# Kernel optimization log

Measured on AMD Instinct MI355X. Metric: run time of the kernel, lower is better.

Reference implementation:

```python
import jax, jax.numpy as jnp
import numpy as np

B, T = 8, 32
DSENS, DA = 512, 32
DS = DE = DIM = 128  # dim_structure = dim_encoded_sensory = memory dim


def l2norm(x, eps=1e-12):
    return x / jnp.maximum(jnp.linalg.norm(x, axis=-1, keepdims=True), eps)


def mlp3(x, W1, b1, W2, b2, W3, b3):
    h = jax.nn.relu(x @ W1 + b1)
    h = jax.nn.relu(h @ W2 + b2)
    return h @ W3 + b3


def mse(a, b):
    return jnp.mean((a - b) ** 2)


def assoc_scan(x, gate, prev):
    # h_t = gate_t * h_{t-1} + x_t with h_0 = prev.  x:[b,t,w], gate:[b,t,1], prev:[b,w]
    x = x.at[:, 0].add(gate[:, 0] * prev)
    def combine(ca, cb):
        ga, xa = ca
        gb, xb = cb
        return ga * gb, xb + gb * xa
    _, h = jax.lax.associative_scan(combine, (gate, x), axis=1)
    return h


def _forward(sensory, actions, enc_w, dec_w, pi_w1, pi_b1, pi_w2, pi_b2, pi_w3, pi_b3,
             rnn_init_hidden, wq, wk, wv, w_hp, m_w1, m_b1, m_w2, m_b2, m_w3, m_b3,
             o_w1, o_b1, o_w2, o_b2, o_w3, o_b3, v_w1, v_b1, v_w2, v_b2, v_w3, v_b3,
             integration_ratio):
    b, t = actions.shape[:2]
    # --- path integration: action MLP -> per-step transition matrices -> sequential RNN scan ---
    trans = mlp3(actions, pi_w1, pi_b1, pi_w2, pi_b2, pi_w3, pi_b3).reshape(b, t, DS, DS)
    h0 = jnp.broadcast_to(l2norm(rnn_init_hidden)[0], (b, DS))
    def step(h, Tm):
        h = l2norm(jax.nn.relu(jnp.einsum('bi,bij->bj', h, Tm)))
        return h, h
    _, hs = jax.lax.scan(step, h0, jnp.moveaxis(trans, 1, 0))
    structural = jnp.moveaxis(hs, 0, 1)                      # [b,t,DS]

    enc = sensory @ enc_w                                    # [b,t,DE]
    meta_p = (m_w1, m_b1, m_w2, m_b2, m_w3, m_b3)

    def retrieve(s, e):
        q = jnp.concatenate([s, e], axis=-1) @ wq            # to_queries
        r = mlp3(q, *meta_p)                                 # meta_memory_mlp (slow copy)
        d = mlp3(r, o_w1, o_b1, o_w2, o_b2, o_w3, o_b3)      # memory_output_decoder
        return d[..., :DS], d[..., DS:]

    dec_gen_s, dec_enc = retrieve(structural, jnp.zeros_like(enc))
    gen_loss = mse(sensory, dec_enc @ dec_w)
    dec_s2, _ = retrieve(jnp.zeros_like(structural), enc)
    relational_loss = 2.0 * mse(dec_s2, structural)          # source computes the identical loss twice
    corr_s, corr_e = retrieve(dec_gen_s, enc)
    sse = jnp.sum((corr_e - enc) ** 2, axis=-1, keepdims=True)
    pred_var = mlp3(jnp.concatenate([corr_s, dec_gen_s, sse], axis=-1),
                    v_w1, v_b1, v_w2, v_b2, v_w3, v_b3)
    inf_s = dec_gen_s + (corr_s - dec_gen_s) * jax.nn.sigmoid(integration_ratio) * pred_var
    consistency_loss = mse(dec_gen_s, inf_s)
    final_s, inf_e = retrieve(inf_s, jnp.zeros_like(enc))
    inf_loss = mse(sensory, inf_e @ dec_w)

    # --- test-time-training memory write: per-sample meta-grads + two assoc scans ---
    joint = jnp.concatenate([final_s, enc], axis=-1)         # [b,t,2*DS]
    keys, values = joint @ wk, joint @ wv                    # [b,t,DIM]
    hp = joint @ w_hp                                        # [b,t,3]
    lr, forget, beta = hp[..., 0], hp[..., 1], hp[..., 2]

    def meta_loss(p, k, v):
        return jnp.mean((mlp3(k, *p) - v) ** 2)
    pb = tuple(jnp.broadcast_to(p, (b,) + p.shape) for p in meta_p)
    grads = jax.vmap(jax.vmap(jax.grad(meta_loss), in_axes=(None, 0, 0)))(pb, keys, values)
    G = jnp.concatenate([g.reshape(b, t, -1) for g in grads], axis=-1)  # [b,t,Wtot]
    W = G.shape[-1]
    p_flat = jnp.broadcast_to(jnp.concatenate([p.ravel() for p in meta_p])[None], (b, W))
    update = assoc_scan(G * lr[..., None], jax.nn.sigmoid(beta)[..., None],
                        jnp.zeros((b, W), G.dtype))          # momentum scan
    acc = assoc_scan(-update, jax.nn.sigmoid(forget)[..., None], p_flat)  # weight-decay scan
    next_state = jnp.concatenate([acc[:, -1], update[:, -1]], axis=-1)    # [b,2W]

    total = gen_loss + relational_loss + consistency_loss + inf_loss
    return jnp.concatenate([jnp.reshape(total, (1,)), next_state.ravel()])


def setup_inputs() -> dict:
    key = jax.random.key(0)
    ks = iter(jax.random.split(key, 48))
    def rn(shape, s=1.0):
        return jax.random.normal(next(ks), shape, dtype=jnp.float32) * s
    def lin(fi, fo):
        return rn((fi, fo), 1.0 / np.sqrt(fi))
    z = lambda n: jnp.zeros((n,), jnp.float32)
    return {
        "sensory": rn((B, T, DSENS)),
        "actions": rn((B, T, DA)),
        "enc_w": lin(DSENS, DE), "dec_w": lin(DE, DSENS),
        "pi_w1": lin(DA, 4 * DA), "pi_b1": z(4 * DA),
        "pi_w2": lin(4 * DA, 4 * DA), "pi_b2": z(4 * DA),
        "pi_w3": lin(4 * DA, DS * DS), "pi_b3": z(DS * DS),
        "rnn_init_hidden": rn((1, DS), 0.01),
        "wq": lin(DS + DE, DIM), "wk": lin(DS + DE, DIM), "wv": lin(DS + DE, DIM),
        "w_hp": lin(DS + DE, 3),
        "m_w1": lin(DIM, 2 * DIM), "m_b1": z(2 * DIM),
        "m_w2": lin(2 * DIM, 2 * DIM), "m_b2": z(2 * DIM),
        "m_w3": lin(2 * DIM, DIM), "m_b3": z(DIM),
        "o_w1": lin(DIM, 2 * DIM), "o_b1": z(2 * DIM),
        "o_w2": lin(2 * DIM, 2 * DIM), "o_b2": z(2 * DIM),
        "o_w3": lin(2 * DIM, DS + DE), "o_b3": z(DS + DE),
        "v_w1": lin(2 * DS + 1, 2 * DS), "v_b1": z(2 * DS),
        "v_w2": lin(2 * DS, 2 * DS), "v_b2": z(2 * DS),
        "v_w3": lin(2 * DS, DS), "v_b3": z(DS),
        "integration_ratio": jnp.zeros((), jnp.float32),
    }


def reference(sensory, actions, enc_w, dec_w, pi_w1, pi_b1, pi_w2, pi_b2, pi_w3, pi_b3,
              rnn_init_hidden, wq, wk, wv, w_hp, m_w1, m_b1, m_w2, m_b2, m_w3, m_b3,
              o_w1, o_b1, o_w2, o_b2, o_w3, o_b3, v_w1, v_b1, v_w2, v_b2, v_w3, v_b3,
              integration_ratio):
    return _forward(sensory, actions, enc_w, dec_w, pi_w1, pi_b1, pi_w2, pi_b2, pi_w3, pi_b3,
                    rnn_init_hidden, wq, wk, wv, w_hp, m_w1, m_b1, m_w2, m_b2, m_w3, m_b3,
                    o_w1, o_b1, o_w2, o_b2, o_w3, o_b3, v_w1, v_b1, v_w2, v_b2, v_w3, v_b3,
                    integration_ratio)
```

## Files before the change

kernel.cpp:

```cpp
#include <hip/hip_runtime.h>
#include <cstdint>
#include <cstddef>

#define DEV __device__ __forceinline__

constexpr size_t W_TOT = 131712;
constexpr size_t OFF_W1 = 0;
constexpr size_t OFF_B1 = 32768;
constexpr size_t OFF_W2 = 33024;
constexpr size_t OFF_B2 = 98560;
constexpr size_t OFF_W3 = 98816;
constexpr size_t OFF_B3 = 131584;

constexpr int OPS = 272;

constexpr size_t P_LOSS = 0;
constexpr size_t P_WA   = 1024;
constexpr size_t P_WU   = 1280;
constexpr size_t P_FT   = 1536;
constexpr size_t P_HP   = 2048;
constexpr size_t P_H2PI = 4096;
constexpr size_t P_ENC  = P_H2PI + 32768;
constexpr size_t P_DGS  = P_ENC + 32768;
constexpr size_t P_INF  = P_DGS + 32768;
constexpr size_t P_KEYS = P_INF + 32768;
constexpr size_t P_VALS = P_KEYS + 32768;
constexpr size_t P_D3   = P_VALS + 32768;
constexpr size_t P_H1   = P_D3 + 32768;
constexpr size_t P_H2   = P_H1 + 65536;
constexpr size_t P_D1   = P_H2 + 65536;
constexpr size_t P_D2   = P_D1 + 65536;
constexpr size_t P_STRUCT = P_D2 + 65536;
constexpr size_t P_TRANS  = P_STRUCT + 32768;

DEV float sigm(float x) { return 1.f / (1.f + expf(-x)); }

DEV float wgsum256(float v, float* red) {
#pragma unroll
  for (int s = 32; s > 0; s >>= 1) v += __shfl_xor(v, s);
  if ((threadIdx.x & 63) == 0) red[threadIdx.x >> 6] = v;
  __syncthreads();
  const float t = red[0] + red[1] + red[2] + red[3];
  __syncthreads();
  return t;
}

template<int K, int OUT, int ROWS>
DEV void denseV4(const float* __restrict__ W, const float* __restrict__ bias,
                 const float* in, int ips, float* out, int ops, int relu,
                 float* scr)
{
  constexpr int OUTG = OUT / 4;
  constexpr int NSEG = 256 / OUTG;
  constexpr int KS = K / NSEG;
  constexpr int NG = KS / 8;
  static_assert(KS % 8 == 0 && NG >= 2, "bad shape");
  const int tid = (int)threadIdx.x;
  const int c = tid & (OUTG - 1);
  const int seg = tid / OUTG;
  const int k0 = seg * KS;
  const float4* W4 = reinterpret_cast<const float4*>(W);
  float4 w0[8], w1[8];
  float acc[ROWS][4];
#pragma unroll
  for (int r = 0; r < ROWS; ++r)
#pragma unroll
    for (int x = 0; x < 4; ++x) acc[r][x] = 0.f;
#pragma unroll
  for (int u = 0; u < 8; ++u) w0[u] = W4[(size_t)(k0 + u) * OUTG + c];
#pragma unroll
  for (int t = 1; t <= NG; ++t) {
    if (t < NG) {
#pragma unroll
      for (int u = 0; u < 8; ++u) w1[u] = W4[(size_t)(k0 + t * 8 + u) * OUTG + c];
    }
#pragma unroll
    for (int u = 0; u < 8; ++u) {
      const int kk = k0 + (t - 1) * 8 + u;
#pragma unroll
      for (int r = 0; r < ROWS; ++r) {
        const float x = in[r * ips + kk];
        acc[r][0] = fmaf(x, w0[u].x, acc[r][0]);
        acc[r][1] = fmaf(x, w0[u].y, acc[r][1]);
        acc[r][2] = fmaf(x, w0[u].z, acc[r][2]);
        acc[r][3] = fmaf(x, w0[u].w, acc[r][3]);
      }
    }
    if (t < NG) {
#pragma unroll
      for (int u = 0; u < 8; ++u) w0[u] = w1[u];
    }
  }
  float4* scr4 = reinterpret_cast<float4*>(scr);
#pragma unroll
  for (int r = 0; r < ROWS; ++r)
    scr4[(seg * ROWS + r) * OUTG + c] =
        make_float4(acc[r][0], acc[r][1], acc[r][2], acc[r][3]);
  __syncthreads();
  for (int idx = tid; idx < OUT * ROWS; idx += 256) {
    const int r = idx / OUT, j = idx % OUT;
    float v = (bias ? bias[j] : 0.f);
#pragma unroll
    for (int s = 0; s < NSEG; ++s) v += scr[(s * ROWS + r) * OUT + j];
    if (relu) v = fmaxf(v, 0.f);
    out[r * ops + j] = v;
  }
  __syncthreads();
}

DEV float declossV4(const float* de, const float* __restrict__ dec_w,
                    const float* sens, float* scr)
{
  const int tid = (int)threadIdx.x;
  const int c = tid & 127;
  const int seg = tid >> 7;
  const int k0 = seg * 64;
  const float4* W4 = reinterpret_cast<const float4*>(dec_w);
  float4 w0[8], w1[8];
  float a[4] = { 0.f, 0.f, 0.f, 0.f };
#pragma unroll
  for (int u = 0; u < 8; ++u) w0[u] = W4[(size_t)(k0 + u) * 128 + c];
#pragma unroll
  for (int t = 1; t <= 8; ++t) {
    if (t < 8) {
#pragma unroll
      for (int u = 0; u < 8; ++u) w1[u] = W4[(size_t)(k0 + t * 8 + u) * 128 + c];
    }
#pragma unroll
    for (int u = 0; u < 8; ++u) {
      const float x = de[k0 + (t - 1) * 8 + u];
      a[0] = fmaf(x, w0[u].x, a[0]);
      a[1] = fmaf(x, w0[u].y, a[1]);
      a[2] = fmaf(x, w0[u].z, a[2]);
      a[3] = fmaf(x, w0[u].w, a[3]);
    }
    if (t < 8) {
#pragma unroll
      for (int u = 0; u < 8; ++u) w0[u] = w1[u];
    }
  }
  float4* scr4 = reinterpret_cast<float4*>(scr);
  scr4[seg * 128 + c] = make_float4(a[0], a[1], a[2], a[3]);
  __syncthreads();
  float lsum = 0.f;
  for (int j = tid; j < 512; j += 256) {
    const float v = scr[j] + scr[512 + j];
    const float d = v - sens[j];
    lsum = fmaf(d, d, lsum);
  }
  __syncthreads();
  return lsum;
}

__global__ __launch_bounds__(128) void k_pi_h2(
    const float* __restrict__ actions,
    const float* __restrict__ w1, const float* __restrict__ b1,
    const float* __restrict__ w2, const float* __restrict__ b2,
    float* __restrict__ h2out)
{
  const int row = blockIdx.x;
  const int j = threadIdx.x;
  __shared__ float a[32];
  __shared__ float h1[128];
  if (j < 32) a[j] = actions[row * 32 + j];
  __syncthreads();
  float acc = b1[j];
#pragma unroll
  for (int i = 0; i < 32; ++i) acc = fmaf(a[i], w1[i * 128 + j], acc);
  h1[j] = fmaxf(acc, 0.f);
  __syncthreads();
  float acc2 = b2[j];
#pragma unroll 8
  for (int i = 0; i < 128; ++i) acc2 = fmaf(h1[i], w2[i * 128 + j], acc2);
  h2out[row * 128 + j] = fmaxf(acc2, 0.f);
}

__global__ __launch_bounds__(256) void k_pi_trans(
    const float* __restrict__ h2,
    const float* __restrict__ w3, const float* __restrict__ b3,
    float* __restrict__ trans)
{
  const int col = blockIdx.x * 256 + threadIdx.x;
  const int r0 = blockIdx.y * 32;
  __shared__ float h2s[32][128];
  for (int idx = threadIdx.x; idx < 32 * 128; idx += 256)
    h2s[idx >> 7][idx & 127] = h2[(size_t)(r0 + (idx >> 7)) * 128 + (idx & 127)];
  __syncthreads();
  float acc[32];
#pragma unroll
  for (int r = 0; r < 32; ++r) acc[r] = 0.f;
  for (int i = 0; i < 128; i += 8) {
    float w[8];
#pragma unroll
    for (int c = 0; c < 8; ++c) w[c] = w3[(size_t)(i + c) * 16384 + col];
#pragma unroll
    for (int r = 0; r < 32; ++r) {
      float s = acc[r];
#pragma unroll
      for (int c = 0; c < 8; ++c) s = fmaf(h2s[r][i + c], w[c], s);
      acc[r] = s;
    }
  }
  const float bv = b3[col];
#pragma unroll
  for (int r = 0; r < 32; ++r)
    trans[(size_t)(r0 + r) * 16384 + col] = acc[r] + bv;
}

__global__ __launch_bounds__(512) void k_rnn(
    const float* __restrict__ trans, const float* __restrict__ rinit,
    float* __restrict__ structural)
{
  const int b = blockIdx.x;
  const int tid = threadIdx.x;
  const int j = tid & 127, seg = tid >> 7;
  __shared__ float h[128];
  __shared__ float part[4][128];
  __shared__ float ssq;
  if (tid < 128) h[tid] = rinit[tid];
  __syncthreads();
  if (tid < 64) {
    float v = h[tid] * h[tid] + h[tid + 64] * h[tid + 64];
#pragma unroll
    for (int s = 32; s > 0; s >>= 1) v += __shfl_xor(v, s);
    if (tid == 0) ssq = v;
  }
  __syncthreads();
  if (tid < 128) h[tid] /= fmaxf(sqrtf(ssq), 1e-12f);
  __syncthreads();

  float cur[32], nxt[32];
  {
    const float* T0 = trans + ((size_t)(b * 32) << 14);
#pragma unroll
    for (int k = 0; k < 32; ++k) cur[k] = T0[(size_t)(seg * 32 + k) * 128 + j];
  }
  for (int t = 0; t < 32; ++t) {
    if (t < 31) {
      const float* Tn = trans + ((size_t)(b * 32 + t + 1) << 14);
#pragma unroll
      for (int k = 0; k < 32; ++k) nxt[k] = Tn[(size_t)(seg * 32 + k) * 128 + j];
    }
    float acc = 0.f;
#pragma unroll
    for (int k = 0; k < 32; ++k) acc = fmaf(h[seg * 32 + k], cur[k], acc);
    part[seg][j] = acc;
    __syncthreads();
    if (tid < 128) {
      float r = fmaxf(part[0][j] + part[1][j] + part[2][j] + part[3][j], 0.f);
      part[0][j] = r;
    }
    __syncthreads();
    if (tid < 64) {
      float v = part[0][tid] * part[0][tid] + part[0][tid + 64] * part[0][tid + 64];
#pragma unroll
      for (int s = 32; s > 0; s >>= 1) v += __shfl_xor(v, s);
      if (tid == 0) ssq = v;
    }
    __syncthreads();
    if (tid < 128) {
      const float nv = part[0][j] / fmaxf(sqrtf(ssq), 1e-12f);
      h[j] = nv;
      structural[(size_t)(b * 32 + t) * 128 + j] = nv;
    }
    __syncthreads();
    if (t < 31) {
#pragma unroll
      for (int k = 0; k < 32; ++k) cur[k] = nxt[k];
    }
  }
}

__global__ __launch_bounds__(256) void kA(
    const float* __restrict__ sensory, const float* __restrict__ structural_,
    const float* __restrict__ enc_w, const float* __restrict__ wq,
    const float* __restrict__ dec_w,
    const float* __restrict__ mw1, const float* __restrict__ mb1,
    const float* __restrict__ mw2, const float* __restrict__ mb2,
    const float* __restrict__ mw3, const float* __restrict__ mb3,
    const float* __restrict__ ow1, const float* __restrict__ ob1,
    const float* __restrict__ ow2, const float* __restrict__ ob2,
    const float* __restrict__ ow3, const float* __restrict__ ob3,
    float* __restrict__ ws_enc, float* __restrict__ ws_dgs,
    float* __restrict__ lossPart)
{
  const int g = blockIdx.x, tid = threadIdx.x;
  __shared__ float sens[512], sRow[128], eRow[128];
  __shared__ float actA[2 * OPS], actB[2 * OPS];
  __shared__ float4 scr4buf[512];
  __shared__ float red[4];
  float* scr = reinterpret_cast<float*>(scr4buf);

  for (int i = tid; i < 512; i += 256) sens[i] = sensory[(size_t)g * 512 + i];
  if (tid < 128) sRow[tid] = structural_[(size_t)g * 128 + tid];
  __syncthreads();

  denseV4<512, 128, 1>(enc_w, nullptr, sens, 0, eRow, 0, 0, scr);
  if (tid < 128) ws_enc[(size_t)g * 128 + tid] = eRow[tid];

  denseV4<128, 128, 1>(wq, nullptr, sRow, 0, actA, 0, 0, scr);
  denseV4<128, 128, 1>(wq + 128 * 128, nullptr, eRow, 0, actA + OPS, 0, 0, scr);
  denseV4<128, 256, 2>(mw1, mb1, actA, OPS, actB, OPS, 1, scr);
  denseV4<256, 256, 2>(mw2, mb2, actB, OPS, actA, OPS, 1, scr);
  denseV4<256, 128, 2>(mw3, mb3, actA, OPS, actB, OPS, 0, scr);
  denseV4<128, 256, 2>(ow1, ob1, actB, OPS, actA, OPS, 1, scr);
  denseV4<256, 256, 2>(ow2, ob2, actA, OPS, actB, OPS, 1, scr);
  denseV4<256, 256, 2>(ow3, ob3, actB, OPS, actA, OPS, 0, scr);
  float lrel = 0.f;
  if (tid < 128) {
    ws_dgs[(size_t)g * 128 + tid] = actA[tid];
    const float d = actA[OPS + tid] - sRow[tid];
    lrel = d * d;
  }
  const float relT = wgsum256(lrel, red);
  if (tid == 0) lossPart[256 + g] = relT;
  const float genT = wgsum256(declossV4(&actA[128], dec_w, sens, scr), red);
  if (tid == 0) lossPart[g] = genT;
}

__global__ __launch_bounds__(256) void kB(
    const float* __restrict__ ws_enc, const float* __restrict__ ws_dgs,
    const float* __restrict__ wq,
    const float* __restrict__ mw1, const float* __restrict__ mb1,
    const float* __restrict__ mw2, const float* __restrict__ mb2,
    const float* __restrict__ mw3, const float* __restrict__ mb3,
    const float* __restrict__ ow1, const float* __restrict__ ob1,
    const float* __restrict__ ow2, const float* __restrict__ ob2,
    const float* __restrict__ ow3, const float* __restrict__ ob3,
    const float* __restrict__ vw1, const float* __restrict__ vb1,
    const float* __restrict__ vw2, const float* __restrict__ vb2,
    const float* __restrict__ vw3, const float* __restrict__ vb3,
    const float* __restrict__ ir,
    float* __restrict__ ws_inf, float* __restrict__ lossPart)
{
  const int g = blockIdx.x, tid = threadIdx.x;
  __shared__ float eRow[128], dgsRow[128], cRow[128];
  __shared__ float cbuf[256];
  __shared__ float actA[2 * OPS], actB[2 * OPS];
  __shared__ float4 scr4buf[512];
  __shared__ float red[4];
  float* scr = reinterpret_cast<float*>(scr4buf);

  if (tid < 128) eRow[tid] = ws_enc[(size_t)g * 128 + tid];
  else dgsRow[tid - 128] = ws_dgs[(size_t)g * 128 + (tid - 128)];
  __syncthreads();

  cbuf[tid] = (tid < 128) ? dgsRow[tid] : eRow[tid - 128];
  __syncthreads();
  denseV4<256, 128, 1>(wq, nullptr, cbuf, 0, actA, 0, 0, scr);
  denseV4<128, 256, 1>(mw1, mb1, actA, 0, actB, 0, 1, scr);
  denseV4<256, 256, 1>(mw2, mb2, actB, 0, actA, 0, 1, scr);
  denseV4<256, 128, 1>(mw3, mb3, actA, 0, actB, 0, 0, scr);
  denseV4<128, 256, 1>(ow1, ob1, actB, 0, actA, 0, 1, scr);
  denseV4<256, 256, 1>(ow2, ob2, actA, 0, actB, 0, 1, scr);
  denseV4<256, 256, 1>(ow3, ob3, actB, 0, actA, 0, 0, scr);
  float ls = 0.f;
  if (tid < 128) {
    cRow[tid] = actA[tid];
    const float d = actA[128 + tid] - eRow[tid];
    ls = d * d;
  }
  const float sseV = wgsum256(ls, red);

  cbuf[tid] = (tid < 128) ? cRow[tid] : dgsRow[tid - 128];
  __syncthreads();
  denseV4<256, 256, 1>(vw1, vb1, cbuf, 0, actB, 0, 0, scr);
  actB[tid] = fmaxf(actB[tid] + sseV * vw1[(size_t)256 * 256 + tid], 0.f);
  __syncthreads();
  denseV4<256, 256, 1>(vw2, vb2, actB, 0, actA, 0, 1, scr);
  denseV4<256, 128, 1>(vw3, vb3, actA, 0, actB, 0, 0, scr);
  const float sig = sigm(ir[0]);
  float lc = 0.f;
  if (tid < 128) {
    const float diff = (cRow[tid] - dgsRow[tid]) * sig * actB[tid];
    ws_inf[(size_t)g * 128 + tid] = dgsRow[tid] + diff;
    lc = diff * diff;
  }
  const float consT = wgsum256(lc, red);
  if (tid == 0) lossPart[512 + g] = consT;
}

__global__ __launch_bounds__(256) void kC(
    const float* __restrict__ sensory,
    const float* __restrict__ ws_enc, const float* __restrict__ ws_inf,
    const float* __restrict__ wq, const float* __restrict__ dec_w,
    const float* __restrict__ mw1, const float* __restrict__ mb1,
    const float* __restrict__ mw2, const float* __restrict__ mb2,
    const float* __restrict__ mw3, const float* __restrict__ mb3,
    const float* __restrict__ ow1, const float* __restrict__ ob1,
    const float* __restrict__ ow2, const float* __restrict__ ob2,
    const float* __restrict__ ow3, const float* __restrict__ ob3,
    const float* __restrict__ wk, const float* __restrict__ wv,
    const float* __restrict__ w_hp,
    float* __restrict__ gKeys, float* __restrict__ gVals,
    float* __restrict__ gHp, float* __restrict__ lossPart)
{
  const int g = blockIdx.x, tid = threadIdx.x;
  __shared__ float sens[512], eRow[128], infRow[128];
  __shared__ float cbuf[256];
  __shared__ float actA[2 * OPS], actB[2 * OPS];
  __shared__ float4 scr4buf[512];
  __shared__ float red[4];
  float* scr = reinterpret_cast<float*>(scr4buf);

  for (int i = tid; i < 512; i += 256) sens[i] = sensory[(size_t)g * 512 + i];
  if (tid < 128) eRow[tid] = ws_enc[(size_t)g * 128 + tid];
  else infRow[tid - 128] = ws_inf[(size_t)g * 128 + (tid - 128)];
  __syncthreads();

  denseV4<128, 128, 1>(wq, nullptr, infRow, 0, actA, 0, 0, scr);
  denseV4<128, 256, 1>(mw1, mb1, actA, 0, actB, 0, 1, scr);
  denseV4<256, 256, 1>(mw2, mb2, actB, 0, actA, 0, 1, scr);
  denseV4<256, 128, 1>(mw3, mb3, actA, 0, actB, 0, 0, scr);
  denseV4<128, 256, 1>(ow1, ob1, actB, 0, actA, 0, 1, scr);
  denseV4<256, 256, 1>(ow2, ob2, actA, 0, actB, 0, 1, scr);
  denseV4<256, 256, 1>(ow3, ob3, actB, 0, actA, 0, 0, scr);
  const float infT = wgsum256(declossV4(&actA[128], dec_w, sens, scr), red);
  if (tid == 0) lossPart[768 + g] = infT;

  cbuf[tid] = (tid < 128) ? actA[tid] : eRow[tid - 128];
  __syncthreads();
  denseV4<256, 128, 1>(wk, nullptr, cbuf, 0, gKeys + (size_t)g * 128, 0, 0, scr);
  denseV4<256, 128, 1>(wv, nullptr, cbuf, 0, gVals + (size_t)g * 128, 0, 0, scr);
  const int c = tid >> 6, l = tid & 63;
  float acc = 0.f;
  if (c < 3) {
    for (int i = l; i < 256; i += 64)
      acc = fmaf(cbuf[i], w_hp[i * 3 + c], acc);
  }
#pragma unroll
  for (int s = 32; s > 0; s >>= 1) acc += __shfl_xor(acc, s);
  if (c < 3 && l == 0) gHp[(size_t)g * 4 + c] = acc;
}

__global__ __launch_bounds__(256) void kD(
    const float* __restrict__ gKeys, const float* __restrict__ gVals,
    const float* __restrict__ gHp,
    const float* __restrict__ mw1, const float* __restrict__ mb1,
    const float* __restrict__ mw2, const float* __restrict__ mb2,
    const float* __restrict__ mw3, const float* __restrict__ mb3,
    float* __restrict__ ws_h1, float* __restrict__ ws_h2,
    float* __restrict__ ws_d1, float* __restrict__ ws_d2, float* __restrict__ ws_d3,
    float* __restrict__ wA, float* __restrict__ wU, float* __restrict__ Ft)
{
  const int tid = threadIdx.x;
  __shared__ float kRow[128], vRow[128];
  __shared__ float actA[256], actB[256], d3R[128], d2R[256];
  __shared__ float4 scr4buf[512];
  __shared__ float lr[256], sf[256], sb[256];
  float* scr = reinterpret_cast<float*>(scr4buf);
  if (blockIdx.x == 256) {
    lr[tid] = gHp[(size_t)tid * 4 + 0];
    sf[tid] = sigm(gHp[(size_t)tid * 4 + 1]);
    sb[tid] = sigm(gHp[(size_t)tid * 4 + 2]);
    __syncthreads();
    if (tid < 8) {
      const int b = tid;
      float cB = 1.f, cF = 1.f, Bv = 1.f;
      wU[b * 32 + 31] = lr[b * 32 + 31];
      wA[b * 32 + 31] = lr[b * 32 + 31];
      for (int t = 30; t >= 0; --t) {
        cB = sb[b * 32 + t + 1] * cB;
        cF = sf[b * 32 + t + 1] * cF;
        Bv = cF + sb[b * 32 + t + 1] * Bv;
        wU[b * 32 + t] = lr[b * 32 + t] * cB;
        wA[b * 32 + t] = lr[b * 32 + t] * Bv;
      }
      float ft = 1.f;
      for (int t = 0; t < 32; ++t) ft *= sf[b * 32 + t];
      Ft[b] = ft;
    }
    return;
  }
  const int g = blockIdx.x;
  if (tid < 128) kRow[tid] = gKeys[(size_t)g * 128 + tid];
  else vRow[tid - 128] = gVals[(size_t)g * 128 + (tid - 128)];
  __syncthreads();
  denseV4<128, 256, 1>(mw1, mb1, kRow, 0, actA, 0, 1, scr);
  ws_h1[(size_t)g * 256 + tid] = actA[tid];
  denseV4<256, 256, 1>(mw2, mb2, actA, 0, actB, 0, 1, scr);
  ws_h2[(size_t)g * 256 + tid] = actB[tid];
  denseV4<256, 128, 1>(mw3, mb3, actB, 0, d3R, 0, 0, scr);
  if (tid < 128) {
    const float d = (d3R[tid] - vRow[tid]) * (2.f / 128.f);
    d3R[tid] = d;
    ws_d3[(size_t)g * 128 + tid] = d;
  }
  __syncthreads();
  {
    const int j = tid;
    float acc = 0.f;
    for (int jc = 0; jc < 128; jc += 4) {
      const float4 w = *reinterpret_cast<const float4*>(&mw3[(size_t)j * 128 + jc]);
      acc = fmaf(w.x, d3R[jc + 0], acc);
      acc = fmaf(w.y, d3R[jc + 1], acc);
      acc = fmaf(w.z, d3R[jc + 2], acc);
      acc = fmaf(w.w, d3R[jc + 3], acc);
    }
    const float v = (actB[j] > 0.f) ? acc : 0.f;
    d2R[j] = v;
    ws_d2[(size_t)g * 256 + j] = v;
  }
  __syncthreads();
  {
    const int j = tid;
    float acc = 0.f;
    for (int jc = 0; jc < 256; jc += 4) {
      const float4 w = *reinterpret_cast<const float4*>(&mw2[(size_t)j * 256 + jc]);
      acc = fmaf(w.x, d2R[jc + 0], acc);
      acc = fmaf(w.y, d2R[jc + 1], acc);
      acc = fmaf(w.z, d2R[jc + 2], acc);
      acc = fmaf(w.w, d2R[jc + 3], acc);
    }
    ws_d1[(size_t)g * 256 + j] = (actA[j] > 0.f) ? acc : 0.f;
  }
}

DEV void outer_body(const float* __restrict__ L, int Lld,
                    const float* __restrict__ D, int Dld,
                    const float* __restrict__ P,
                    const float* __restrict__ wA, const float* __restrict__ wU,
                    const float* __restrict__ Ftot,
                    float* __restrict__ out, size_t regionOff, int J,
                    int b, int i0, float* __restrict__ wAk, float* __restrict__ wUk)
{
  const int tid = threadIdx.x;
  for (int idx = tid; idx < 1024; idx += 256) {
    const int t = idx >> 5, ii = idx & 31;
    const float kv = L[(size_t)(b * 32 + t) * Lld + i0 + ii];
    wAk[t * 33 + ii] = wA[b * 32 + t] * kv;
    wUk[t * 33 + ii] = wU[b * 32 + t] * kv;
  }
  __syncthreads();
  const int j = (J == 256) ? tid : (tid & 127);
  const int g2 = (J == 256) ? 0 : (tid >> 7);
  const int span = (J == 256) ? 32 : 16;
  const int iBeg = g2 * span;
  float dv[32];
#pragma unroll
  for (int t = 0; t < 32; ++t) dv[t] = D[(size_t)(b * 32 + t) * Dld + j];
  const float ft = Ftot[b];
  float* ob = out + 1 + (size_t)b * (2 * W_TOT);
  for (int ii = iBeg; ii < iBeg + span; ++ii) {
    float aA = 0.f, aU = 0.f;
#pragma unroll
    for (int t = 0; t < 32; ++t) {
      aA = fmaf(wAk[t * 33 + ii], dv[t], aA);
      aU = fmaf(wUk[t * 33 + ii], dv[t], aU);
    }
    const int i = i0 + ii;
    const size_t w = regionOff + (size_t)i * J + j;
    ob[w] = ft * P[(size_t)i * J + j] - aA;
    ob[W_TOT + w] = aU;
  }
}

__global__ __launch_bounds__(256) void kW(
    const float* __restrict__ keys, const float* __restrict__ h1,
    const float* __restrict__ h2, const float* __restrict__ d1,
    const float* __restrict__ d2, const float* __restrict__ d3,
    const float* __restrict__ mw1, const float* __restrict__ mb1,
    const float* __restrict__ mw2, const float* __restrict__ mb2,
    const float* __restrict__ mw3, const float* __restrict__ mb3,
    const float* __restrict__ wA, const float* __restrict__ wU,
    const float* __restrict__ Ft, const float* __restrict__ lossPart,
    float* __restrict__ out)
{
  __shared__ float wAk[32 * 33], wUk[32 * 33];
  __shared__ float red[4];
  const int bid = blockIdx.x;
  const int tid = threadIdx.x;
  if (bid < 32) {
    outer_body(keys, 128, d1, 256, mw1, wA, wU, Ft, out, OFF_W1, 256,
               bid >> 2, (bid & 3) * 32, wAk, wUk);
  } else if (bid < 96) {
    const int x = bid - 32;
    outer_body(h1, 256, d2, 256, mw2, wA, wU, Ft, out, OFF_W2, 256,
               x >> 3, (x & 7) * 32, wAk, wUk);
  } else if (bid < 160) {
    const int x = bid - 96;
    outer_body(h2, 256, d3, 128, mw3, wA, wU, Ft, out, OFF_W3, 128,
               x >> 3, (x & 7) * 32, wAk, wUk);
  } else if (bid < 168) {
    const int b = bid - 160;
    const float ft = Ft[b];
    float* ob = out + 1 + (size_t)b * (2 * W_TOT);
    for (int idx = tid; idx < 640; idx += 256) {
      const float* D; int ld, j; size_t off; float pv;
      if (idx < 256)      { D = d1; ld = 256; j = idx;       off = OFF_B1; pv = mb1[j]; }
      else if (idx < 512) { D = d2; ld = 256; j = idx - 256; off = OFF_B2; pv = mb2[j]; }
      else                { D = d3; ld = 128; j = idx - 512; off = OFF_B3; pv = mb3[j]; }
      float aA = 0.f, aU = 0.f;
#pragma unroll
      for (int t = 0; t < 32; ++t) {
        const float dv = D[(size_t)(b * 32 + t) * ld + j];
        aA = fmaf(wA[b * 32 + t], dv, aA);
        aU = fmaf(wU[b * 32 + t], dv, aU);
      }
      ob[off + j] = ft * pv - aA;
      ob[W_TOT + off + j] = aU;
    }
  } else {
    const int c = tid >> 6, l = tid & 63;
    float v = lossPart[c * 256 + l] + lossPart[c * 256 + 64 + l] +
              lossPart[c * 256 + 128 + l] + lossPart[c * 256 + 192 + l];
#pragma unroll
    for (int s = 32; s > 0; s >>= 1) v += __shfl_xor(v, s);
    if (l == 0) red[c] = v;
    __syncthreads();
    if (tid == 0) {
      const float i1 = 1.f / (256.f * 512.f);
      const float i2 = 1.f / (256.f * 128.f);
      out[0] = red[0] * i1 + 2.f * red[1] * i2 + red[2] * i2 + red[3] * i1;
    }
  }
}

extern "C" void kernel_launch(void* const* d_in, const int* in_sizes, int n_in,
                              void* d_out, int out_size, void* d_ws, size_t ws_size,
                              hipStream_t stream)
{
  const float* sensory = (const float*)d_in[0];
  const float* actions = (const float*)d_in[1];
  const float* enc_w = (const float*)d_in[2];
  const float* dec_w = (const float*)d_in[3];
  const float* pi_w1 = (const float*)d_in[4];
  const float* pi_b1 = (const float*)d_in[5];
  const float* pi_w2 = (const float*)d_in[6];
  const float* pi_b2 = (const float*)d_in[7];
  const float* pi_w3 = (const float*)d_in[8];
  const float* pi_b3 = (const float*)d_in[9];
  const float* rinit = (const float*)d_in[10];
  const float* wq = (const float*)d_in[11];
  const float* wk = (const float*)d_in[12];
  const float* wv = (const float*)d_in[13];
  const float* w_hp = (const float*)d_in[14];
  const float* mw1 = (const float*)d_in[15]; const float* mb1 = (const float*)d_in[16];
  const float* mw2 = (const float*)d_in[17]; const float* mb2 = (const float*)d_in[18];
  const float* mw3 = (const float*)d_in[19]; const float* mb3 = (const float*)d_in[20];
  const float* ow1 = (const float*)d_in[21]; const float* ob1 = (const float*)d_in[22];
  const float* ow2 = (const float*)d_in[23]; const float* ob2 = (const float*)d_in[24];
  const float* ow3 = (const float*)d_in[25]; const float* ob3 = (const float*)d_in[26];
  const float* vw1 = (const float*)d_in[27]; const float* vb1 = (const float*)d_in[28];
  const float* vw2 = (const float*)d_in[29]; const float* vb2 = (const float*)d_in[30];
  const float* vw3 = (const float*)d_in[31]; const float* vb3 = (const float*)d_in[32];
  const float* ir  = (const float*)d_in[33];

  float* ws  = (float*)d_ws;
  float* out = (float*)d_out;

  float* lossP = ws + P_LOSS;
  float* wA = ws + P_WA; float* wU = ws + P_WU; float* Ft = ws + P_FT;
  float* hp = ws + P_HP;
  float* h2pi = ws + P_H2PI;
  float* enc = ws + P_ENC;
  float* dgs = ws + P_DGS;
  float* inf = ws + P_INF;
  float* keys = ws + P_KEYS;
  float* vals = ws + P_VALS;
  float* d3s = ws + P_D3;
  float* h1s = ws + P_H1;
  float* h2s = ws + P_H2;
  float* d1s = ws + P_D1;
  float* d2s = ws + P_D2;
  float* structural = ws + P_STRUCT;
  float* trans = ws + P_TRANS;

  hipLaunchKernelGGL(k_pi_h2, dim3(256), dim3(128), 0, stream,
                     actions, pi_w1, pi_b1, pi_w2, pi_b2, h2pi);
  hipLaunchKernelGGL(k_pi_trans, dim3(64, 8), dim3(256), 0, stream,
                     h2pi, pi_w3, pi_b3, trans);
  hipLaunchKernelGGL(k_rnn, dim3(8), dim3(512), 0, stream, trans, rinit, structural);
  hipLaunchKernelGGL(kA, dim3(256), dim3(256), 0, stream,
                     sensory, structural, enc_w, wq, dec_w,
                     mw1, mb1, mw2, mb2, mw3, mb3,
                     ow1, ob1, ow2, ob2, ow3, ob3,
                     enc, dgs, lossP);
  hipLaunchKernelGGL(kB, dim3(256), dim3(256), 0, stream,
                     enc, dgs, wq,
                     mw1, mb1, mw2, mb2, mw3, mb3,
                     ow1, ob1, ow2, ob2, ow3, ob3,
                     vw1, vb1, vw2, vb2, vw3, vb3,
                     ir, inf, lossP);
  hipLaunchKernelGGL(kC, dim3(256), dim3(256), 0, stream,
                     sensory, enc, inf, wq, dec_w,
                     mw1, mb1, mw2, mb2, mw3, mb3,
                     ow1, ob1, ow2, ob2, ow3, ob3,
                     wk, wv, w_hp, keys, vals, hp, lossP);
  hipLaunchKernelGGL(kD, dim3(257), dim3(256), 0, stream,
                     keys, vals, hp, mw1, mb1, mw2, mb2, mw3, mb3,
                     h1s, h2s, d1s, d2s, d3s, wA, wU, Ft);
  hipLaunchKernelGGL(kW, dim3(169), dim3(256), 0, stream,
                     keys, h1s, h2s, d1s, d2s, d3s,
                     mw1, mb1, mw2, mb2, mw3, mb3,
                     wA, wU, Ft, lossP, out);
}
```

Measured before the change: 202.0 us.

## Widen dense tiles to 8 outputs per thread, double RNN block, prefetch trans weights

The dense helper now has each thread compute two float4 output groups (8 columns), which halves threads per K-segment and doubles the number of K-segments; the scratch buffers are enlarged to match. The separate decoder-loss routine is replaced by the generic dense helper with a 512-wide output. The RNN scan kernel moves to 1024 threads with 16 rows per thread to shorten each step's serial dot product, and the transition-matrix kernel gains register double-buffering of weight loads. Risks include higher register pressure in the dense routine, more partial sums in the reduction, and extra synchronisation cost from the larger RNN block.

```diff
diff --git a/kernel.cpp b/kernel.cpp
--- a/kernel.cpp
+++ b/kernel.cpp
@@ -46,33 +46,41 @@
 }
 
 template<int K, int OUT, int ROWS>
-DEV void denseV4(const float* __restrict__ W, const float* __restrict__ bias,
-                 const float* in, int ips, float* out, int ops, int relu,
-                 float* scr)
+DEV void denseW(const float* __restrict__ W, const float* __restrict__ bias,
+                const float* in, int ips, float* out, int ops, int relu,
+                float* scr)
 {
   constexpr int OUTG = OUT / 4;
-  constexpr int NSEG = 256 / OUTG;
-  constexpr int KS = K / NSEG;
-  constexpr int NG = KS / 8;
-  static_assert(KS % 8 == 0 && NG >= 2, "bad shape");
+  constexpr int HALF = OUTG / 2;
+  constexpr int TPS  = HALF;
+  constexpr int NSEG = 256 / TPS;
+  constexpr int KS   = K / NSEG;
+  constexpr int NG   = KS / 8;
+  static_assert(KS % 8 == 0 && NG >= 1, "bad shape");
   const int tid = (int)threadIdx.x;
-  const int c = tid & (OUTG - 1);
-  const int seg = tid / OUTG;
-  const int k0 = seg * KS;
+  const int c   = tid & (TPS - 1);
+  const int seg = tid / TPS;
+  const int k0  = seg * KS;
   const float4* W4 = reinterpret_cast<const float4*>(W);
-  float4 w0[8], w1[8];
-  float acc[ROWS][4];
+  float4 a0[8], b0[8], a1[8], b1[8];
+  float acc[ROWS][8];
 #pragma unroll
   for (int r = 0; r < ROWS; ++r)
 #pragma unroll
-    for (int x = 0; x < 4; ++x) acc[r][x] = 0.f;
-#pragma unroll
-  for (int u = 0; u < 8; ++u) w0[u] = W4[(size_t)(k0 + u) * OUTG + c];
+    for (int x = 0; x < 8; ++x) acc[r][x] = 0.f;
+#pragma unroll
+  for (int u = 0; u < 8; ++u) {
+    a0[u] = W4[(size_t)(k0 + u) * OUTG + c];
+    b0[u] = W4[(size_t)(k0 + u) * OUTG + c + HALF];
+  }
 #pragma unroll
   for (int t = 1; t <= NG; ++t) {
     if (t < NG) {
 #pragma unroll
-      for (int u = 0; u < 8; ++u) w1[u] = W4[(size_t)(k0 + t * 8 + u) * OUTG + c];
+      for (int u = 0; u < 8; ++u) {
+        a1[u] = W4[(size_t)(k0 + t * 8 + u) * OUTG + c];
+        b1[u] = W4[(size_t)(k0 + t * 8 + u) * OUTG + c + HALF];
+      }
     }
 #pragma unroll
     for (int u = 0; u < 8; ++u) {
@@ -80,22 +88,29 @@
 #pragma unroll
       for (int r = 0; r < ROWS; ++r) {
         const float x = in[r * ips + kk];
-        acc[r][0] = fmaf(x, w0[u].x, acc[r][0]);
-        acc[r][1] = fmaf(x, w0[u].y, acc[r][1]);
-        acc[r][2] = fmaf(x, w0[u].z, acc[r][2]);
-        acc[r][3] = fmaf(x, w0[u].w, acc[r][3]);
+        acc[r][0] = fmaf(x, a0[u].x, acc[r][0]);
+        acc[r][1] = fmaf(x, a0[u].y, acc[r][1]);
+        acc[r][2] = fmaf(x, a0[u].z, acc[r][2]);
+        acc[r][3] = fmaf(x, a0[u].w, acc[r][3]);
+        acc[r][4] = fmaf(x, b0[u].x, acc[r][4]);
+        acc[r][5] = fmaf(x, b0[u].y, acc[r][5]);
+        acc[r][6] = fmaf(x, b0[u].z, acc[r][6]);
+        acc[r][7] = fmaf(x, b0[u].w, acc[r][7]);
       }
     }
     if (t < NG) {
 #pragma unroll
-      for (int u = 0; u < 8; ++u) w0[u] = w1[u];
-    }
-  }
-  float4* scr4 = reinterpret_cast<float4*>(scr);
-#pragma unroll
-  for (int r = 0; r < ROWS; ++r)
-    scr4[(seg * ROWS + r) * OUTG + c] =
+      for (int u = 0; u < 8; ++u) { a0[u] = a1[u]; b0[u] = b1[u]; }
+    }
+  }
+  float4* s4 = reinterpret_cast<float4*>(scr);
+#pragma unroll
+  for (int r = 0; r < ROWS; ++r) {
+    s4[(seg * ROWS + r) * OUTG + c] =
         make_float4(acc[r][0], acc[r][1], acc[r][2], acc[r][3]);
+    s4[(seg * ROWS + r) * OUTG + c + HALF] =
+        make_float4(acc[r][4], acc[r][5], acc[r][6], acc[r][7]);
+  }
   __syncthreads();
   for (int idx = tid; idx < OUT * ROWS; idx += 256) {
     const int r = idx / OUT, j = idx % OUT;
@@ -106,50 +121,6 @@
     out[r * ops + j] = v;
   }
   __syncthreads();
-}
-
-DEV float declossV4(const float* de, const float* __restrict__ dec_w,
-                    const float* sens, float* scr)
-{
-  const int tid = (int)threadIdx.x;
-  const int c = tid & 127;
-  const int seg = tid >> 7;
-  const int k0 = seg * 64;
-  const float4* W4 = reinterpret_cast<const float4*>(dec_w);
-  float4 w0[8], w1[8];
-  float a[4] = { 0.f, 0.f, 0.f, 0.f };
-#pragma unroll
-  for (int u = 0; u < 8; ++u) w0[u] = W4[(size_t)(k0 + u) * 128 + c];
-#pragma unroll
-  for (int t = 1; t <= 8; ++t) {
-    if (t < 8) {
-#pragma unroll
-      for (int u = 0; u < 8; ++u) w1[u] = W4[(size_t)(k0 + t * 8 + u) * 128 + c];
-    }
-#pragma unroll
-    for (int u = 0; u < 8; ++u) {
-      const float x = de[k0 + (t - 1) * 8 + u];
-      a[0] = fmaf(x, w0[u].x, a[0]);
-      a[1] = fmaf(x, w0[u].y, a[1]);
-      a[2] = fmaf(x, w0[u].z, a[2]);
-      a[3] = fmaf(x, w0[u].w, a[3]);
-    }
-    if (t < 8) {
-#pragma unroll
-      for (int u = 0; u < 8; ++u) w0[u] = w1[u];
-    }
-  }
-  float4* scr4 = reinterpret_cast<float4*>(scr);
-  scr4[seg * 128 + c] = make_float4(a[0], a[1], a[2], a[3]);
-  __syncthreads();
-  float lsum = 0.f;
-  for (int j = tid; j < 512; j += 256) {
-    const float v = scr[j] + scr[512 + j];
-    const float d = v - sens[j];
-    lsum = fmaf(d, d, lsum);
-  }
-  __syncthreads();
-  return lsum;
 }
 
 __global__ __launch_bounds__(128) void k_pi_h2(
@@ -189,16 +160,25 @@
   float acc[32];
 #pragma unroll
   for (int r = 0; r < 32; ++r) acc[r] = 0.f;
-  for (int i = 0; i < 128; i += 8) {
-    float w[8];
-#pragma unroll
-    for (int c = 0; c < 8; ++c) w[c] = w3[(size_t)(i + c) * 16384 + col];
+  float w0[8], w1[8];
+#pragma unroll
+  for (int c = 0; c < 8; ++c) w0[c] = w3[(size_t)c * 16384 + col];
+#pragma unroll
+  for (int i = 8; i <= 128; i += 8) {
+    if (i < 128) {
+#pragma unroll
+      for (int c = 0; c < 8; ++c) w1[c] = w3[(size_t)(i + c) * 16384 + col];
+    }
 #pragma unroll
     for (int r = 0; r < 32; ++r) {
       float s = acc[r];
 #pragma unroll
-      for (int c = 0; c < 8; ++c) s = fmaf(h2s[r][i + c], w[c], s);
+      for (int c = 0; c < 8; ++c) s = fmaf(h2s[r][i - 8 + c], w0[c], s);
       acc[r] = s;
+    }
+    if (i < 128) {
+#pragma unroll
+      for (int c = 0; c < 8; ++c) w0[c] = w1[c];
     }
   }
   const float bv = b3[col];
@@ -207,7 +187,7 @@
     trans[(size_t)(r0 + r) * 16384 + col] = acc[r] + bv;
 }
 
-__global__ __launch_bounds__(512) void k_rnn(
+__global__ __launch_bounds__(1024) void k_rnn(
     const float* __restrict__ trans, const float* __restrict__ rinit,
     float* __restrict__ structural)
 {
@@ -215,7 +195,7 @@
   const int tid = threadIdx.x;
   const int j = tid & 127, seg = tid >> 7;
   __shared__ float h[128];
-  __shared__ float part[4][128];
+  __shared__ float part[8][128];
   __shared__ float ssq;
   if (tid < 128) h[tid] = rinit[tid];
   __syncthreads();
@@ -229,26 +209,28 @@
   if (tid < 128) h[tid] /= fmaxf(sqrtf(ssq), 1e-12f);
   __syncthreads();
 
-  float cur[32], nxt[32];
+  float cur[16], nxt[16];
   {
     const float* T0 = trans + ((size_t)(b * 32) << 14);
 #pragma unroll
-    for (int k = 0; k < 32; ++k) cur[k] = T0[(size_t)(seg * 32 + k) * 128 + j];
+    for (int k = 0; k < 16; ++k) cur[k] = T0[(size_t)(seg * 16 + k) * 128 + j];
   }
   for (int t = 0; t < 32; ++t) {
     if (t < 31) {
       const float* Tn = trans + ((size_t)(b * 32 + t + 1) << 14);
 #pragma unroll
-      for (int k = 0; k < 32; ++k) nxt[k] = Tn[(size_t)(seg * 32 + k) * 128 + j];
+      for (int k = 0; k < 16; ++k) nxt[k] = Tn[(size_t)(seg * 16 + k) * 128 + j];
     }
     float acc = 0.f;
 #pragma unroll
-    for (int k = 0; k < 32; ++k) acc = fmaf(h[seg * 32 + k], cur[k], acc);
+    for (int k = 0; k < 16; ++k) acc = fmaf(h[seg * 16 + k], cur[k], acc);
     part[seg][j] = acc;
     __syncthreads();
     if (tid < 128) {
-      float r = fmaxf(part[0][j] + part[1][j] + part[2][j] + part[3][j], 0.f);
-      part[0][j] = r;
+      float r = part[0][j];
+#pragma unroll
+      for (int s = 1; s < 8; ++s) r += part[s][j];
+      part[0][j] = fmaxf(r, 0.f);
     }
     __syncthreads();
     if (tid < 64) {
@@ -266,7 +248,7 @@
     __syncthreads();
     if (t < 31) {
 #pragma unroll
-      for (int k = 0; k < 32; ++k) cur[k] = nxt[k];
+      for (int k = 0; k < 16; ++k) cur[k] = nxt[k];
     }
   }
 }
@@ -287,7 +269,7 @@
   const int g = blockIdx.x, tid = threadIdx.x;
   __shared__ float sens[512], sRow[128], eRow[128];
   __shared__ float actA[2 * OPS], actB[2 * OPS];
-  __shared__ float4 scr4buf[512];
+  __shared__ float4 scr4buf[1024];
   __shared__ float red[4];
   float* scr = reinterpret_cast<float*>(scr4buf);
 
@@ -295,17 +277,17 @@
   if (tid < 128) sRow[tid] = structural_[(size_t)g * 128 + tid];
   __syncthreads();
 
-  denseV4<512, 128, 1>(enc_w, nullptr, sens, 0, eRow, 0, 0, scr);
+  denseW<512, 128, 1>(enc_w, nullptr, sens, 0, eRow, 0, 0, scr);
   if (tid < 128) ws_enc[(size_t)g * 128 + tid] = eRow[tid];
 
-  denseV4<128, 128, 1>(wq, nullptr, sRow, 0, actA, 0, 0, scr);
-  denseV4<128, 128, 1>(wq + 128 * 128, nullptr, eRow, 0, actA + OPS, 0, 0, scr);
-  denseV4<128, 256, 2>(mw1, mb1, actA, OPS, actB, OPS, 1, scr);
-  denseV4<256, 256, 2>(mw2, mb2, actB, OPS, actA, OPS, 1, scr);
-  denseV4<256, 128, 2>(mw3, mb3, actA, OPS, actB, OPS, 0, scr);
-  denseV4<128, 256, 2>(ow1, ob1, actB, OPS, actA, OPS, 1, scr);
-  denseV4<256, 256, 2>(ow2, ob2, actA, OPS, actB, OPS, 1, scr);
-  denseV4<256, 256, 2>(ow3, ob3, actB, OPS, actA, OPS, 0, scr);
+  denseW<128, 128, 1>(wq, nullptr, sRow, 0, actA, 0, 0, scr);
+  denseW<128, 128, 1>(wq + 128 * 128, nullptr, eRow, 0, actA + OPS, 0, 0, scr);
+  denseW<128, 256, 2>(mw1, mb1, actA, OPS, actB, OPS, 1, scr);
+  denseW<256, 256, 2>(mw2, mb2, actB, OPS, actA, OPS, 1, scr);
+  denseW<256, 128, 2>(mw3, mb3, actA, OPS, actB, OPS, 0, scr);
+  denseW<128, 256, 2>(ow1, ob1, actB, OPS, actA, OPS, 1, scr);
+  denseW<256, 256, 2>(ow2, ob2, actA, OPS, actB, OPS, 1, scr);
+  denseW<256, 256, 2>(ow3, ob3, actB, OPS, actA, OPS, 0, scr);
   float lrel = 0.f;
   if (tid < 128) {
     ws_dgs[(size_t)g * 128 + tid] = actA[tid];
@@ -314,8 +296,16 @@
   }
   const float relT = wgsum256(lrel, red);
   if (tid == 0) lossPart[256 + g] = relT;
-  const float genT = wgsum256(declossV4(&actA[128], dec_w, sens, scr), red);
-  if (tid == 0) lossPart[g] = genT;
+  denseW<128, 512, 1>(dec_w, nullptr, &actA[128], 0, actB, 0, 0, scr);
+  {
+    float ls = 0.f;
+    for (int j2 = tid; j2 < 512; j2 += 256) {
+      const float d = actB[j2] - sens[j2];
+      ls = fmaf(d, d, ls);
+    }
+    const float genT = wgsum256(ls, red);
+    if (tid == 0) lossPart[g] = genT;
+  }
 }
 
 __global__ __launch_bounds__(256) void kB(
@@ -337,7 +327,7 @@
   __shared__ float eRow[128], dgsRow[128], cRow[128];
   __shared__ float cbuf[256];
   __shared__ float actA[2 * OPS], actB[2 * OPS];
-  __shared__ float4 scr4buf[512];
+  __shared__ float4 scr4buf[1024];
   __shared__ float red[4];
   float* scr = reinterpret_cast<float*>(scr4buf);
 
@@ -347,13 +337,13 @@
 
   cbuf[tid] = (tid < 128) ? dgsRow[tid] : eRow[tid - 128];
   __syncthreads();
-  denseV4<256, 128, 1>(wq, nullptr, cbuf, 0, actA, 0, 0, scr);
-  denseV4<128, 256, 1>(mw1, mb1, actA, 0, actB, 0, 1, scr);
-  denseV4<256, 256, 1>(mw2, mb2, actB, 0, actA, 0, 1, scr);
-  denseV4<256, 128, 1>(mw3, mb3, actA, 0, actB, 0, 0, scr);
-  denseV4<128, 256, 1>(ow1, ob1, actB, 0, actA, 0, 1, scr);
-  denseV4<256, 256, 1>(ow2, ob2, actA, 0, actB, 0, 1, scr);
-  denseV4<256, 256, 1>(ow3, ob3, actB, 0, actA, 0, 0, scr);
+  denseW<256, 128, 1>(wq, nullptr, cbuf, 0, actA, 0, 0, scr);
+  denseW<128, 256, 1>(mw1, mb1, actA, 0, actB, 0, 1, scr);
+  denseW<256, 256, 1>(mw2, mb2, actB, 0, actA, 0, 1, scr);
+  denseW<256, 128, 1>(mw3, mb3, actA, 0, actB, 0, 0, scr);
+  denseW<128, 256, 1>(ow1, ob1, actB, 0, actA, 0, 1, scr);
+  denseW<256, 256, 1>(ow2, ob2, actA, 0, actB, 0, 1, scr);
+  denseW<256, 256, 1>(ow3, ob3, actB, 0, actA, 0, 0, scr);
   float ls = 0.f;
   if (tid < 128) {
     cRow[tid] = actA[tid];
@@ -364,11 +354,11 @@
 
   cbuf[tid] = (tid < 128) ? cRow[tid] : dgsRow[tid - 128];
   __syncthreads();
-  denseV4<256, 256, 1>(vw1, vb1, cbuf, 0, actB, 0, 0, scr);
+  denseW<256, 256, 1>(vw1, vb1, cbuf, 0, actB, 0, 0, scr);
   actB[tid] = fmaxf(actB[tid] + sseV * vw1[(size_t)256 * 256 + tid], 0.f);
   __syncthreads();
-  denseV4<256, 256, 1>(vw2, vb2, actB, 0, actA, 0, 1, scr);
-  denseV4<256, 128, 1>(vw3, vb3, actA, 0, actB, 0, 0, scr);
+  denseW<256, 256, 1>(vw2, vb2, actB, 0, actA, 0, 1, scr);
+  denseW<256, 128, 1>(vw3, vb3, actA, 0, actB, 0, 0, scr);
   const float sig = sigm(ir[0]);
   float lc = 0.f;
   if (tid < 128) {
@@ -399,7 +389,7 @@
   __shared__ float sens[512], eRow[128], infRow[128];
   __shared__ float cbuf[256];
   __shared__ float actA[2 * OPS], actB[2 * OPS];
-  __shared__ float4 scr4buf[512];
+  __shared__ float4 scr4buf[1024];
   __shared__ float red[4];
   float* scr = reinterpret_cast<float*>(scr4buf);
 
@@ -408,20 +398,29 @@
   else infRow[tid - 128] = ws_inf[(size_t)g * 128 + (tid - 128)];
   __syncthreads();
 
-  denseV4<128, 128, 1>(wq, nullptr, infRow, 0, actA, 0, 0, scr);
-  denseV4<128, 256, 1>(mw1, mb1, actA, 0, actB, 0, 1, scr);
-  denseV4<256, 256, 1>(mw2, mb2, actB, 0, actA, 0, 1, scr);
-  denseV4<256, 128, 1>(mw3, mb3, actA, 0, actB, 0, 0, scr);
-  denseV4<128, 256, 1>(ow1, ob1, actB, 0, actA, 0, 1, scr);
-  denseV4<256, 256, 1>(ow2, ob2, actA, 0, actB, 0, 1, scr);
-  denseV4<256, 256, 1>(ow3, ob3, actB, 0, actA, 0, 0, scr);
-  const float infT = wgsum256(declossV4(&actA[128], dec_w, sens, scr), red);
-  if (tid == 0) lossPart[768 + g] = infT;
+  denseW<128, 128, 1>(wq, nullptr, infRow, 0, actA, 0, 0, scr);
+  denseW<128, 256, 1>(mw1, mb1, actA, 0, actB, 0, 1, scr);
+  denseW<256, 256, 1>(mw2, mb2, actB, 0, actA, 0, 1, scr);
+  denseW<256, 128, 1>(mw3, mb3, actA, 0, actB, 0, 0, scr);
+  denseW<128, 256, 1>(ow1, ob1, actB, 0, actA, 0, 1, scr);
+  denseW<256, 256, 1>(ow2, ob2, actA, 0, actB, 0, 1, scr);
+  denseW<256, 256, 1>(ow3, ob3, actB, 0, actA, 0, 0, scr);
+  denseW<128, 512, 1>(dec_w, nullptr, &actA[128], 0, actB, 0, 0, scr);
+  {
+    float ls = 0.f;
+    for (int j2 = tid; j2 < 512; j2 += 256) {
+      const float d = actB[j2] - sens[j2];
+      ls = fmaf(d, d, ls);
+    }
+    const float infT = wgsum256(ls, red);
+    if (tid == 0) lossPart[768 + g] = infT;
+  }
+  __syncthreads();
 
   cbuf[tid] = (tid < 128) ? actA[tid] : eRow[tid - 128];
   __syncthreads();
-  denseV4<256, 128, 1>(wk, nullptr, cbuf, 0, gKeys + (size_t)g * 128, 0, 0, scr);
-  denseV4<256, 128, 1>(wv, nullptr, cbuf, 0, gVals + (size_t)g * 128, 0, 0, scr);
+  denseW<256, 128, 1>(wk, nullptr, cbuf, 0, gKeys + (size_t)g * 128, 0, 0, scr);
+  denseW<256, 128, 1>(wv, nullptr, cbuf, 0, gVals + (size_t)g * 128, 0, 0, scr);
   const int c = tid >> 6, l = tid & 63;
   float acc = 0.f;
   if (c < 3) {
@@ -446,7 +445,7 @@
   const int tid = threadIdx.x;
   __shared__ float kRow[128], vRow[128];
   __shared__ float actA[256], actB[256], d3R[128], d2R[256];
-  __shared__ float4 scr4buf[512];
+  __shared__ float4 scr4buf[1024];
   __shared__ float lr[256], sf[256], sb[256];
   float* scr = reinterpret_cast<float*>(scr4buf);
   if (blockIdx.x == 256) {
@@ -476,11 +475,11 @@
   if (tid < 128) kRow[tid] = gKeys[(size_t)g * 128 + tid];
   else vRow[tid - 128] = gVals[(size_t)g * 128 + (tid - 128)];
   __syncthreads();
-  denseV4<128, 256, 1>(mw1, mb1, kRow, 0, actA, 0, 1, scr);
+  denseW<128, 256, 1>(mw1, mb1, kRow, 0, actA, 0, 1, scr);
   ws_h1[(size_t)g * 256 + tid] = actA[tid];
-  denseV4<256, 256, 1>(mw2, mb2, actA, 0, actB, 0, 1, scr);
+  denseW<256, 256, 1>(mw2, mb2, actA, 0, actB, 0, 1, scr);
   ws_h2[(size_t)g * 256 + tid] = actB[tid];
-  denseV4<256, 128, 1>(mw3, mb3, actB, 0, d3R, 0, 0, scr);
+  denseW<256, 128, 1>(mw3, mb3, actB, 0, d3R, 0, 0, scr);
   if (tid < 128) {
     const float d = (d3R[tid] - vRow[tid]) * (2.f / 128.f);
     d3R[tid] = d;
@@ -670,7 +669,7 @@
                      actions, pi_w1, pi_b1, pi_w2, pi_b2, h2pi);
   hipLaunchKernelGGL(k_pi_trans, dim3(64, 8), dim3(256), 0, stream,
                      h2pi, pi_w3, pi_b3, trans);
-  hipLaunchKernelGGL(k_rnn, dim3(8), dim3(512), 0, stream, trans, rinit, structural);
+  hipLaunchKernelGGL(k_rnn, dim3(8), dim3(1024), 0, stream, trans, rinit, structural);
   hipLaunchKernelGGL(kA, dim3(256), dim3(256), 0, stream,
                      sensory, structural, enc_w, wq, dec_w,
                      mw1, mb1, mw2, mb2, mw3, mb3,
```

Result: faster. 193.2 us (-4.4%).
